# Optimization experiments

Measured on AMD Instinct MI355X. Metric: run time of the kernel, lower is better.

The kernel has to match this reference:

```python
import jax, jax.numpy as jnp
import numpy as np

N = 100000   # nodes
E = 640000   # edges
IN = 256     # raw input feature dim
D = 128      # post-MLP node feature dim (fixed in FilterGNN)


def setup_inputs() -> dict:
    key = jax.random.key(0)
    ks = jax.random.split(key, 10)
    x = jax.random.normal(ks[0], (N, IN), jnp.float32)
    alpha = jax.random.uniform(ks[1], (E, 1), jnp.float32)  # edge gate logits in [0,1)
    edge_index = jax.random.randint(ks[2], (2, E), 0, N, dtype=jnp.int32)
    norm = jnp.ones((E,), jnp.float32)  # passed to message in the original but unused
    # MLP `lin`: in_channels -> 512 -> 256 -> 128 (kaiming-normal weights, zero bias)
    def kaiming(k, fan_out, fan_in):
        return jax.random.normal(k, (fan_out, fan_in), jnp.float32) * jnp.sqrt(2.0 / fan_in)
    W1 = kaiming(ks[3], 512, IN); b1 = jnp.zeros((512,), jnp.float32)
    W2 = kaiming(ks[4], 256, 512); b2 = jnp.zeros((256,), jnp.float32)
    W3 = kaiming(ks[5], D, 256);  b3 = jnp.zeros((D,), jnp.float32)
    return {"x": x, "alpha": alpha, "edge_index": edge_index, "norm": norm,
            "W1": W1, "b1": b1, "W2": W2, "b2": b2, "W3": W3, "b3": b3}


def reference(x, alpha, edge_index, norm, W1, b1, W2, b2, W3, b3):
    # FilterGNN.lin: Linear-Tanh-Linear-Tanh-Linear  -> [N, 128]
    h = jnp.tanh(x @ W1.T + b1)
    h = jnp.tanh(h @ W2.T + b2)
    h = h @ W3.T + b3
    # FilterGraphConv1: gather x_j, elementwise relu gate, scatter-mean over targets.
    # (The [-1, H, C] view with H*C = 128 is a pure reshape; the gate broadcasts
    #  over all features, so the math is identical without the head split.)
    src, dst = edge_index[0], edge_index[1]
    gate = 2.0 * jax.nn.relu(jax.lax.stop_gradient(alpha) - 0.5)  # [E, 1]
    msg = h[src] * gate                                           # [E, 128] gather + gate
    sums = jax.ops.segment_sum(msg, dst, num_segments=N)          # [N, 128]
    cnt = jax.ops.segment_sum(jnp.ones((E,), h.dtype), dst, num_segments=N)
    out = sums / jnp.maximum(cnt, 1.0)[:, None]                   # scatter-mean (0 if no edges)
    return out
```

## Files before the change

### kernel.cpp

```cpp
#include <hip/hip_runtime.h>

typedef __attribute__((ext_vector_type(8))) short short8;
typedef __attribute__((ext_vector_type(4))) float f32x4;

__device__ __forceinline__ unsigned short f2bf(float f) {
    union { float f; unsigned u; } v; v.f = f;
    unsigned r = v.u + 0x7FFFu + ((v.u >> 16) & 1u);
    return (unsigned short)(r >> 16);
}
__device__ __forceinline__ float bf2f(unsigned short h) {
    union { unsigned u; float f; } v; v.u = ((unsigned)h) << 16;
    return v.f;
}

__device__ __forceinline__ float tanh_fast(float x) {
    float xc = fminf(fmaxf(x, -9.0f), 9.0f);
    float t  = __expf(2.0f * xc);
    return (t - 1.0f) * __builtin_amdgcn_rcpf(t + 1.0f);
}

#define GLD16(gptr, lptr)                                                     \
    __builtin_amdgcn_global_load_lds(                                         \
        (const __attribute__((address_space(1))) unsigned int*)(gptr),        \
        (__attribute__((address_space(3))) unsigned int*)(lptr), 16, 0, 0)

__global__ __launch_bounds__(256) void cast_f32_bf16(
    const float* __restrict__ src, unsigned short* __restrict__ dst, int n)
{
    int t = (blockIdx.x * 256 + threadIdx.x) * 4;
    if (t >= n) return;
    float4 v = *(const float4*)(src + t);
    unsigned long long p =
        (unsigned long long)f2bf(v.x)
      | ((unsigned long long)f2bf(v.y) << 16)
      | ((unsigned long long)f2bf(v.z) << 32)
      | ((unsigned long long)f2bf(v.w) << 48);
    *(unsigned long long*)(dst + t) = p;
}

#define TM 128
#define TN 128
#define BK 64

template<bool TANH>
__global__ __launch_bounds__(256) void gemm_bt(
    const unsigned short* __restrict__ A, const unsigned short* __restrict__ B,
    const float* __restrict__ bias, unsigned short* __restrict__ C,
    int M, int N, int K)
{
    __shared__ __align__(16) short As[TM][BK];
    __shared__ __align__(16) short Bs[TN][BK];

    const int tid  = threadIdx.x;
    const int wave = tid >> 6;
    const int lane = tid & 63;
    const int m0 = blockIdx.x * TM;
    const int n0 = blockIdx.y * TN;
    const int wm = (wave >> 1) * 64;
    const int wn = (wave & 1) * 64;
    const int lm = lane & 15;
    const int quad = lane >> 4;

    const int srow = lane >> 3;
    const int scol = ((lane & 7) ^ srow) * 8;

    const int cc0 = (quad ^ (lm & 7)) * 8;
    const int cc1 = ((4 + quad) ^ (lm & 7)) * 8;

    f32x4 acc[4][4] = {};

    for (int k0 = 0; k0 < K; k0 += BK) {
        #pragma unroll
        for (int i = 0; i < 4; ++i) {
            int row = wave * 32 + i * 8;
            int gr = m0 + row + srow; if (gr >= M) gr = M - 1;
            GLD16(A + (size_t)gr * K + k0 + scol, &As[row][0]);
            GLD16(B + (size_t)(n0 + row + srow) * K + k0 + scol, &Bs[row][0]);
        }
        __syncthreads();

        #pragma unroll
        for (int ks = 0; ks < BK; ks += 32) {
            const int cc = (ks == 0) ? cc0 : cc1;
            short8 af[4], bf_[4];
            #pragma unroll
            for (int i = 0; i < 4; ++i) {
                af[i]  = *(const short8*)&As[wm + i * 16 + lm][cc];
                bf_[i] = *(const short8*)&Bs[wn + i * 16 + lm][cc];
            }
            #pragma unroll
            for (int im = 0; im < 4; ++im)
                #pragma unroll
                for (int in = 0; in < 4; ++in)
                    acc[im][in] = __builtin_amdgcn_mfma_f32_16x16x32_bf16(
                        af[im], bf_[in], acc[im][in], 0, 0, 0);
        }
        __syncthreads();
    }

    #pragma unroll
    for (int im = 0; im < 4; ++im) {
        int gm_base = m0 + wm + im * 16 + quad * 4;
        #pragma unroll
        for (int in = 0; in < 4; ++in) {
            int gn = n0 + wn + in * 16 + lm;
            float bv = bias[gn];
            #pragma unroll
            for (int r = 0; r < 4; ++r) {
                int gm = gm_base + r;
                if (gm < M) {
                    float v = acc[im][in][r] + bv;
                    if (TANH) v = tanh_fast(v);
                    C[(size_t)gm * N + gn] = f2bf(v);
                }
            }
        }
    }
}

__global__ __launch_bounds__(256) void edge_hist(
    const int* __restrict__ ei, const float* __restrict__ alpha,
    unsigned long long* __restrict__ deg, int E)
{
    int e = blockIdx.x * 256 + threadIdx.x;
    if (e >= E) return;
    int dst = ei[E + e];
    float gate = 2.0f * fmaxf(alpha[e] - 0.5f, 0.0f);
    atomicAdd(&deg[dst], 0x100000000ULL | (gate > 0.0f ? 1ULL : 0ULL));
}

__global__ __launch_bounds__(256) void scan1(
    const unsigned long long* __restrict__ deg, int* __restrict__ rowptr,
    int* __restrict__ partials, int N)
{
    __shared__ int sums[256];
    int base = blockIdx.x * 1024 + threadIdx.x * 4;
    int v[4];
    #pragma unroll
    for (int i = 0; i < 4; ++i) {
        int idx = base + i;
        v[i] = (idx < N) ? (int)(deg[idx] & 0xffffffffULL) : 0;
    }
    int s = v[0] + v[1] + v[2] + v[3];
    sums[threadIdx.x] = s;
    __syncthreads();
    for (int off = 1; off < 256; off <<= 1) {
        int t = (threadIdx.x >= off) ? sums[threadIdx.x - off] : 0;
        __syncthreads();
        sums[threadIdx.x] += t;
        __syncthreads();
    }
    int excl = sums[threadIdx.x] - s;
    if (threadIdx.x == 255) partials[blockIdx.x] = sums[255];
    int run = excl;
    #pragma unroll
    for (int i = 0; i < 4; ++i) {
        int idx = base + i;
        if (idx < N) rowptr[idx] = run;
        run += v[i];
    }
}

__global__ __launch_bounds__(256) void scan2(int* __restrict__ partials, int nb)
{
    __shared__ int s[256];
    int v = (threadIdx.x < nb) ? partials[threadIdx.x] : 0;
    s[threadIdx.x] = v;
    __syncthreads();
    for (int off = 1; off < 256; off <<= 1) {
        int t = (threadIdx.x >= off) ? s[threadIdx.x - off] : 0;
        __syncthreads();
        s[threadIdx.x] += t;
        __syncthreads();
    }
    partials[threadIdx.x] = s[threadIdx.x] - v;
}

__global__ __launch_bounds__(256) void scan3(
    int* __restrict__ rowptr, int* __restrict__ cursor,
    const int* __restrict__ partials, int N)
{
    int i = blockIdx.x * 256 + threadIdx.x;
    if (i >= N) return;
    int r = rowptr[i] + partials[i >> 10];
    rowptr[i] = r;
    cursor[i] = r;
}

__global__ __launch_bounds__(256) void edge_fill(
    const int* __restrict__ ei, const float* __restrict__ alpha,
    int* __restrict__ cursor, int2* __restrict__ recs, int E)
{
    int e = blockIdx.x * 256 + threadIdx.x;
    if (e >= E) return;
    float gate = 2.0f * fmaxf(alpha[e] - 0.5f, 0.0f);
    if (gate > 0.0f) {
        int dst = ei[E + e];
        int src = ei[e];
        int pos = atomicAdd(&cursor[dst], 1);
        recs[pos] = make_int2(src, __float_as_int(gate));
    }
}

__global__ __launch_bounds__(256) void node_gather(
    const unsigned short* __restrict__ h, const unsigned long long* __restrict__ deg,
    const int* __restrict__ rowptr, const int2* __restrict__ recs,
    float* __restrict__ out, int N)
{
    int wave = threadIdx.x >> 6;
    int lane = threadIdx.x & 63;
    int node = blockIdx.x * 4 + wave;
    if (node >= N) return;
    unsigned long long d = deg[node];
    int dAll  = __builtin_amdgcn_readfirstlane((int)(d >> 32));
    int dG    = __builtin_amdgcn_readfirstlane((int)(d & 0xffffffffULL));
    int start = __builtin_amdgcn_readfirstlane(rowptr[node]);
    float ax = 0.0f, ay = 0.0f;
    for (int j = 0; j < dG; ++j) {
        int2 rec = recs[start + j];
        float gate = __int_as_float(rec.y);
        unsigned u = *(const unsigned*)(h + ((size_t)rec.x << 7) + lane * 2);
        ax += bf2f((unsigned short)(u & 0xffffu)) * gate;
        ay += bf2f((unsigned short)(u >> 16)) * gate;
    }
    float inv = 1.0f / fmaxf((float)dAll, 1.0f);
    *(float2*)(out + ((size_t)node << 7) + lane * 2) = make_float2(ax * inv, ay * inv);
}

extern "C" void kernel_launch(void* const* d_in, const int* in_sizes, int n_in,
                              void* d_out, int out_size, void* d_ws, size_t ws_size,
                              hipStream_t stream) {
    const float* x     = (const float*)d_in[0];
    const float* alpha = (const float*)d_in[1];
    const int*   ei    = (const int*)d_in[2];
    const float* W1 = (const float*)d_in[4];
    const float* b1 = (const float*)d_in[5];
    const float* W2 = (const float*)d_in[6];
    const float* b2 = (const float*)d_in[7];
    const float* W3 = (const float*)d_in[8];
    const float* b3 = (const float*)d_in[9];
    float* out = (float*)d_out;

    const int N = in_sizes[0] / 256;
    const int E = in_sizes[1];
    const int IN = 256, H1 = 512, H2 = 256, D = 128;

    char* ws = (char*)d_ws;
    size_t off = 0;
    auto take = [&](size_t bytes) { char* p = ws + off; off = (off + bytes + 255) & ~(size_t)255; return p; };
    unsigned short* xbf  = (unsigned short*)take((size_t)N * IN * 2);
    unsigned short* h1bf = (unsigned short*)take((size_t)N * H1 * 2);
    unsigned short* hbf  = (unsigned short*)take((size_t)N * D  * 2);
    unsigned short* w1bf = (unsigned short*)take((size_t)H1 * IN * 2);
    unsigned short* w2bf = (unsigned short*)take((size_t)H2 * H1 * 2);
    unsigned short* w3bf = (unsigned short*)take((size_t)D  * H2 * 2);
    unsigned short* h2bf = xbf;

    char* cbase = (char*)h1bf;
    size_t coff = 0;
    auto ctake = [&](size_t bytes) { char* p = cbase + coff; coff = (coff + bytes + 255) & ~(size_t)255; return p; };
    unsigned long long* deg = (unsigned long long*)ctake((size_t)N * 8);
    int*  rowptr   = (int*)ctake((size_t)N * 4);
    int*  cursor   = (int*)ctake((size_t)N * 4);
    int*  partials = (int*)ctake(256 * 4);
    int2* recs     = (int2*)ctake((size_t)E * 8);

    cast_f32_bf16<<<(N * IN / 4 + 255) / 256, 256, 0, stream>>>(x,  xbf,  N * IN);
    cast_f32_bf16<<<(H1 * IN / 4 + 255) / 256, 256, 0, stream>>>(W1, w1bf, H1 * IN);
    cast_f32_bf16<<<(H2 * H1 / 4 + 255) / 256, 256, 0, stream>>>(W2, w2bf, H2 * H1);
    cast_f32_bf16<<<(D * H2 / 4 + 255) / 256, 256, 0, stream>>>(W3, w3bf, D * H2);

    const int mblk = (N + TM - 1) / TM;
    dim3 blk(256);
    gemm_bt<true ><<<dim3(mblk, H1 / TN), blk, 0, stream>>>(xbf,  w1bf, b1, h1bf, N, H1, IN);
    gemm_bt<true ><<<dim3(mblk, H2 / TN), blk, 0, stream>>>(h1bf, w2bf, b2, h2bf, N, H2, H1);
    gemm_bt<false><<<dim3(mblk, D / TN),  blk, 0, stream>>>(h2bf, w3bf, b3, hbf,  N, D,  H2);

    hipMemsetAsync(deg, 0, (size_t)N * 8, stream);
    edge_hist<<<(E + 255) / 256, blk, 0, stream>>>(ei, alpha, deg, E);
    const int nb1 = (N + 1023) / 1024;
    scan1<<<nb1, blk, 0, stream>>>(deg, rowptr, partials, N);
    scan2<<<1, blk, 0, stream>>>(partials, nb1);
    scan3<<<(N + 255) / 256, blk, 0, stream>>>(rowptr, cursor, partials, N);
    edge_fill<<<(E + 255) / 256, blk, 0, stream>>>(ei, alpha, cursor, recs, E);

    node_gather<<<(N + 3) / 4, blk, 0, stream>>>(hbf, deg, rowptr, recs, out, N);
}
```

Measured before the change: 436.8 us.

## Fuse input cast into first GEMM, merge weight casts, drop scan3, widen gather

The first GEMM now loads fp32 x directly into LDS and converts it to bf16 by truncation when building fragments. This removes the separate cast kernel and its write and read of a bf16 copy of x. The three weight casts become one launch, and scan3 is removed by adding the block partial offset inside edge_fill and node_gather. node_gather now processes two edges per wave iteration, each half-wave covering all 128 features, and combines the halves with a shuffle. The trade-offs are twice the LDS for the A tile, truncation instead of round-to-nearest for x, and an extra workspace buffer for h2.

```diff
diff --git a/kernel.cpp b/kernel.cpp
--- a/kernel.cpp
+++ b/kernel.cpp
@@ -24,32 +24,41 @@
         (const __attribute__((address_space(1))) unsigned int*)(gptr),        \
         (__attribute__((address_space(3))) unsigned int*)(lptr), 16, 0, 0)
 
-__global__ __launch_bounds__(256) void cast_f32_bf16(
-    const float* __restrict__ src, unsigned short* __restrict__ dst, int n)
+__device__ __forceinline__ unsigned pk_trunc(float lo, float hi) {
+    return __builtin_amdgcn_perm(__float_as_uint(hi), __float_as_uint(lo), 0x07060302u);
+}
+
+__global__ __launch_bounds__(256) void cast_weights(
+    const float* __restrict__ W1, const float* __restrict__ W2,
+    const float* __restrict__ W3, unsigned short* __restrict__ w1bf,
+    unsigned short* __restrict__ w2bf, unsigned short* __restrict__ w3bf)
 {
     int t = (blockIdx.x * 256 + threadIdx.x) * 4;
-    if (t >= n) return;
-    float4 v = *(const float4*)(src + t);
+    const float* s; unsigned short* d; int base;
+    if (t < 131072)      { s = W1; d = w1bf; base = t; }
+    else if (t < 262144) { s = W2; d = w2bf; base = t - 131072; }
+    else if (t < 294912) { s = W3; d = w3bf; base = t - 262144; }
+    else return;
+    float4 v = *(const float4*)(s + base);
     unsigned long long p =
         (unsigned long long)f2bf(v.x)
       | ((unsigned long long)f2bf(v.y) << 16)
       | ((unsigned long long)f2bf(v.z) << 32)
       | ((unsigned long long)f2bf(v.w) << 48);
-    *(unsigned long long*)(dst + t) = p;
+    *(unsigned long long*)(d + base) = p;
 }
 
 #define TM 128
 #define TN 128
 #define BK 64
 
-template<bool TANH>
-__global__ __launch_bounds__(256) void gemm_bt(
-    const unsigned short* __restrict__ A, const unsigned short* __restrict__ B,
+__global__ __launch_bounds__(256) void gemm_a32_bt(
+    const float* __restrict__ A, const unsigned short* __restrict__ B,
     const float* __restrict__ bias, unsigned short* __restrict__ C,
     int M, int N, int K)
 {
-    __shared__ __align__(16) short As[TM][BK];
-    __shared__ __align__(16) short Bs[TN][BK];
+    __shared__ __align__(16) float Asf[TM][BK];
+    __shared__ __align__(16) short Bs[TM][BK];
 
     const int tid  = threadIdx.x;
     const int wave = tid >> 6;
@@ -61,9 +70,96 @@
     const int lm = lane & 15;
     const int quad = lane >> 4;
 
+    const int srowA = lane >> 4;
+    const int lA    = lane & 15;
+    const int srowB = lane >> 3;
+    const int cB    = ((lane & 7) ^ srowB) * 8;
+
+    f32x4 acc[4][4] = {};
+
+    for (int k0 = 0; k0 < K; k0 += BK) {
+        #pragma unroll
+        for (int i = 0; i < 8; ++i) {
+            int row0 = wave * 32 + i * 4;
+            int gr = m0 + row0 + srowA; if (gr >= M) gr = M - 1;
+            int cA = lA ^ ((row0 + srowA) & 15);
+            GLD16(A + (size_t)gr * K + k0 + cA * 4, &Asf[row0][0]);
+        }
+        #pragma unroll
+        for (int i = 0; i < 4; ++i) {
+            int row0 = wave * 32 + i * 8;
+            GLD16(B + (size_t)(n0 + row0 + srowB) * K + k0 + cB, &Bs[row0][0]);
+        }
+        __syncthreads();
+
+        #pragma unroll
+        for (int ks = 0; ks < BK; ks += 32) {
+            const int qb = ks >> 2;
+            const int ccB = (((ks >> 3) + quad) ^ (lm & 7)) * 8;
+            short8 af[4], bfr[4];
+            #pragma unroll
+            for (int i = 0; i < 4; ++i) {
+                const float* rowp = &Asf[wm + i * 16 + lm][0];
+                float4 f0 = *(const float4*)(rowp + (((qb + quad * 2)     ) ^ lm) * 4);
+                float4 f1 = *(const float4*)(rowp + (((qb + quad * 2) + 1) ^ lm) * 4);
+                union { short8 s; uint4 u; } cv;
+                cv.u.x = pk_trunc(f0.x, f0.y);
+                cv.u.y = pk_trunc(f0.z, f0.w);
+                cv.u.z = pk_trunc(f1.x, f1.y);
+                cv.u.w = pk_trunc(f1.z, f1.w);
+                af[i]  = cv.s;
+                bfr[i] = *(const short8*)&Bs[wn + i * 16 + lm][ccB];
+            }
+            #pragma unroll
+            for (int im = 0; im < 4; ++im)
+                #pragma unroll
+                for (int in = 0; in < 4; ++in)
+                    acc[im][in] = __builtin_amdgcn_mfma_f32_16x16x32_bf16(
+                        af[im], bfr[in], acc[im][in], 0, 0, 0);
+        }
+        __syncthreads();
+    }
+
+    #pragma unroll
+    for (int im = 0; im < 4; ++im) {
+        int gm_base = m0 + wm + im * 16 + quad * 4;
+        #pragma unroll
+        for (int in = 0; in < 4; ++in) {
+            int gn = n0 + wn + in * 16 + lm;
+            float bv = bias[gn];
+            #pragma unroll
+            for (int r = 0; r < 4; ++r) {
+                int gm = gm_base + r;
+                if (gm < M) {
+                    float v = tanh_fast(acc[im][in][r] + bv);
+                    C[(size_t)gm * N + gn] = f2bf(v);
+                }
+            }
+        }
+    }
+}
+
+template<bool TANH>
+__global__ __launch_bounds__(256) void gemm_bt(
+    const unsigned short* __restrict__ A, const unsigned short* __restrict__ B,
+    const float* __restrict__ bias, unsigned short* __restrict__ C,
+    int M, int N, int K)
+{
+    __shared__ __align__(16) short As[TM][BK];
+    __shared__ __align__(16) short Bs[TM][BK];
+
+    const int tid  = threadIdx.x;
+    const int wave = tid >> 6;
+    const int lane = tid & 63;
+    const int m0 = blockIdx.x * TM;
+    const int n0 = blockIdx.y * TN;
+    const int wm = (wave >> 1) * 64;
+    const int wn = (wave & 1) * 64;
+    const int lm = lane & 15;
+    const int quad = lane >> 4;
+
     const int srow = lane >> 3;
     const int scol = ((lane & 7) ^ srow) * 8;
-
     const int cc0 = (quad ^ (lm & 7)) * 8;
     const int cc1 = ((4 + quad) ^ (lm & 7)) * 8;
 
@@ -131,7 +227,7 @@
 
 __global__ __launch_bounds__(256) void scan1(
     const unsigned long long* __restrict__ deg, int* __restrict__ rowptr,
-    int* __restrict__ partials, int N)
+    int* __restrict__ cursor, int* __restrict__ partials, int N)
 {
     __shared__ int sums[256];
     int base = blockIdx.x * 1024 + threadIdx.x * 4;
@@ -156,7 +252,7 @@
     #pragma unroll
     for (int i = 0; i < 4; ++i) {
         int idx = base + i;
-        if (idx < N) rowptr[idx] = run;
+        if (idx < N) { rowptr[idx] = run; cursor[idx] = run; }
         run += v[i];
     }
 }
@@ -176,20 +272,10 @@
     partials[threadIdx.x] = s[threadIdx.x] - v;
 }
 
-__global__ __launch_bounds__(256) void scan3(
-    int* __restrict__ rowptr, int* __restrict__ cursor,
-    const int* __restrict__ partials, int N)
-{
-    int i = blockIdx.x * 256 + threadIdx.x;
-    if (i >= N) return;
-    int r = rowptr[i] + partials[i >> 10];
-    rowptr[i] = r;
-    cursor[i] = r;
-}
-
 __global__ __launch_bounds__(256) void edge_fill(
     const int* __restrict__ ei, const float* __restrict__ alpha,
-    int* __restrict__ cursor, int2* __restrict__ recs, int E)
+    int* __restrict__ cursor, const int* __restrict__ partials,
+    int2* __restrict__ recs, int E)
 {
     int e = blockIdx.x * 256 + threadIdx.x;
     if (e >= E) return;
@@ -197,15 +283,15 @@
     if (gate > 0.0f) {
         int dst = ei[E + e];
         int src = ei[e];
-        int pos = atomicAdd(&cursor[dst], 1);
+        int pos = atomicAdd(&cursor[dst], 1) + partials[dst >> 10];
         recs[pos] = make_int2(src, __float_as_int(gate));
     }
 }
 
 __global__ __launch_bounds__(256) void node_gather(
     const unsigned short* __restrict__ h, const unsigned long long* __restrict__ deg,
-    const int* __restrict__ rowptr, const int2* __restrict__ recs,
-    float* __restrict__ out, int N)
+    const int* __restrict__ rowptr, const int* __restrict__ partials,
+    const int2* __restrict__ recs, float* __restrict__ out, int N)
 {
     int wave = threadIdx.x >> 6;
     int lane = threadIdx.x & 63;
@@ -214,17 +300,29 @@
     unsigned long long d = deg[node];
     int dAll  = __builtin_amdgcn_readfirstlane((int)(d >> 32));
     int dG    = __builtin_amdgcn_readfirstlane((int)(d & 0xffffffffULL));
-    int start = __builtin_amdgcn_readfirstlane(rowptr[node]);
-    float ax = 0.0f, ay = 0.0f;
-    for (int j = 0; j < dG; ++j) {
-        int2 rec = recs[start + j];
-        float gate = __int_as_float(rec.y);
-        unsigned u = *(const unsigned*)(h + ((size_t)rec.x << 7) + lane * 2);
-        ax += bf2f((unsigned short)(u & 0xffffu)) * gate;
-        ay += bf2f((unsigned short)(u >> 16)) * gate;
-    }
-    float inv = 1.0f / fmaxf((float)dAll, 1.0f);
-    *(float2*)(out + ((size_t)node << 7) + lane * 2) = make_float2(ax * inv, ay * inv);
+    int start = __builtin_amdgcn_readfirstlane(rowptr[node] + partials[node >> 10]);
+    int half = lane >> 5, hl = lane & 31;
+    float ax = 0.f, ay = 0.f, az = 0.f, aw = 0.f;
+    for (int j = 0; j < dG; j += 2) {
+        int jj = j + half;
+        int idx = start + (jj < dG ? jj : dG - 1);
+        int2 rec = recs[idx];
+        float gate = (jj < dG) ? __int_as_float(rec.y) : 0.0f;
+        uint2 u = *(const uint2*)(h + ((size_t)rec.x << 7) + hl * 4);
+        ax += bf2f((unsigned short)(u.x & 0xffffu)) * gate;
+        ay += bf2f((unsigned short)(u.x >> 16)) * gate;
+        az += bf2f((unsigned short)(u.y & 0xffffu)) * gate;
+        aw += bf2f((unsigned short)(u.y >> 16)) * gate;
+    }
+    ax += __shfl_down(ax, 32);
+    ay += __shfl_down(ay, 32);
+    az += __shfl_down(az, 32);
+    aw += __shfl_down(aw, 32);
+    if (half == 0) {
+        float inv = 1.0f / fmaxf((float)dAll, 1.0f);
+        *(float4*)(out + ((size_t)node << 7) + hl * 4) =
+            make_float4(ax * inv, ay * inv, az * inv, aw * inv);
+    }
 }
 
 extern "C" void kernel_launch(void* const* d_in, const int* in_sizes, int n_in,
@@ -248,13 +346,12 @@
     char* ws = (char*)d_ws;
     size_t off = 0;
     auto take = [&](size_t bytes) { char* p = ws + off; off = (off + bytes + 255) & ~(size_t)255; return p; };
-    unsigned short* xbf  = (unsigned short*)take((size_t)N * IN * 2);
     unsigned short* h1bf = (unsigned short*)take((size_t)N * H1 * 2);
+    unsigned short* h2bf = (unsigned short*)take((size_t)N * H2 * 2);
     unsigned short* hbf  = (unsigned short*)take((size_t)N * D  * 2);
     unsigned short* w1bf = (unsigned short*)take((size_t)H1 * IN * 2);
     unsigned short* w2bf = (unsigned short*)take((size_t)H2 * H1 * 2);
     unsigned short* w3bf = (unsigned short*)take((size_t)D  * H2 * 2);
-    unsigned short* h2bf = xbf;
 
     char* cbase = (char*)h1bf;
     size_t coff = 0;
@@ -265,24 +362,21 @@
     int*  partials = (int*)ctake(256 * 4);
     int2* recs     = (int2*)ctake((size_t)E * 8);
 
-    cast_f32_bf16<<<(N * IN / 4 + 255) / 256, 256, 0, stream>>>(x,  xbf,  N * IN);
-    cast_f32_bf16<<<(H1 * IN / 4 + 255) / 256, 256, 0, stream>>>(W1, w1bf, H1 * IN);
-    cast_f32_bf16<<<(H2 * H1 / 4 + 255) / 256, 256, 0, stream>>>(W2, w2bf, H2 * H1);
-    cast_f32_bf16<<<(D * H2 / 4 + 255) / 256, 256, 0, stream>>>(W3, w3bf, D * H2);
+    dim3 blk(256);
+
+    cast_weights<<<(294912 / 4 + 255) / 256, blk, 0, stream>>>(W1, W2, W3, w1bf, w2bf, w3bf);
 
     const int mblk = (N + TM - 1) / TM;
-    dim3 blk(256);
-    gemm_bt<true ><<<dim3(mblk, H1 / TN), blk, 0, stream>>>(xbf,  w1bf, b1, h1bf, N, H1, IN);
-    gemm_bt<true ><<<dim3(mblk, H2 / TN), blk, 0, stream>>>(h1bf, w2bf, b2, h2bf, N, H2, H1);
-    gemm_bt<false><<<dim3(mblk, D / TN),  blk, 0, stream>>>(h2bf, w3bf, b3, hbf,  N, D,  H2);
+    gemm_a32_bt    <<<dim3(mblk, H1 / TN), blk, 0, stream>>>(x,    w1bf, b1, h1bf, N, H1, IN);
+    gemm_bt<true > <<<dim3(mblk, H2 / TN), blk, 0, stream>>>(h1bf, w2bf, b2, h2bf, N, H2, H1);
+    gemm_bt<false> <<<dim3(mblk, D / TN),  blk, 0, stream>>>(h2bf, w3bf, b3, hbf,  N, D,  H2);
 
     hipMemsetAsync(deg, 0, (size_t)N * 8, stream);
     edge_hist<<<(E + 255) / 256, blk, 0, stream>>>(ei, alpha, deg, E);
     const int nb1 = (N + 1023) / 1024;
-    scan1<<<nb1, blk, 0, stream>>>(deg, rowptr, partials, N);
+    scan1<<<nb1, blk, 0, stream>>>(deg, rowptr, cursor, partials, N);
     scan2<<<1, blk, 0, stream>>>(partials, nb1);
-    scan3<<<(N + 255) / 256, blk, 0, stream>>>(rowptr, cursor, partials, N);
-    edge_fill<<<(E + 255) / 256, blk, 0, stream>>>(ei, alpha, cursor, recs, E);
-
-    node_gather<<<(N + 3) / 4, blk, 0, stream>>>(hbf, deg, rowptr, recs, out, N);
-}
+    edge_fill<<<(E + 255) / 256, blk, 0, stream>>>(ei, alpha, cursor, partials, recs, E);
+
+    node_gather<<<(N + 3) / 4, blk, 0, stream>>>(hbf, deg, rowptr, partials, recs, out, N);
+}
```

Measured after the change: 441.1 us. About the same (+1.0%).
